# Optimization experiments

Hardware: AMD Instinct MI355X
Metric: run time of the kernel (lower is better)

The kernel has to match this reference:

```python
import jax, jax.numpy as jnp
import numpy as np

N, E = 50000, 800000
F_IN, F_OUT, H, F_EDGE = 256, 32, 8, 5
LEAKY_SLOPE = 0.2


def setup_inputs() -> dict:
    key = jax.random.key(0)
    ks = jax.random.split(key, 6)
    x = jax.random.normal(ks[0], (N, F_IN), dtype=jnp.float32)
    edge_index = jax.random.randint(ks[1], (2, E), 0, N, dtype=jnp.int64)
    edge_attr = jax.random.normal(ks[2], (E, F_EDGE), dtype=jnp.float32)
    degree_src = jax.random.randint(ks[3], (E,), 0, 64, dtype=jnp.int64)
    # Xavier-uniform params
    lim_W = float(np.sqrt(6.0 / (F_IN + F_OUT)))
    W = jax.random.uniform(ks[4], (H, F_IN, F_OUT), minval=-lim_W, maxval=lim_W, dtype=jnp.float32)
    A = 2 * F_OUT + F_EDGE
    lim_a = float(np.sqrt(6.0 / (H + A)))
    a = jax.random.uniform(ks[5], (H, A), minval=-lim_a, maxval=lim_a, dtype=jnp.float32)
    lim_e = float(np.sqrt(1.0 / F_EDGE))
    W_edge_w = jax.random.uniform(jax.random.fold_in(key, 7), (F_EDGE, F_EDGE), minval=-lim_e, maxval=lim_e, dtype=jnp.float32)
    return {"x": x, "edge_index": edge_index, "edge_attr": edge_attr,
            "degree_src": degree_src, "W": W, "a": a, "W_edge_w": W_edge_w}


def reference(x, edge_index, edge_attr, degree_src, W, a, W_edge_w):
    n = x.shape[0]
    h, f_out = W.shape[0], W.shape[2]
    src, dst = edge_index[0], edge_index[1]
    # per-head projection: (N, H, F_out)
    Wh = jnp.einsum('nf,hfo->nho', x, W)
    # split attention vector instead of materializing the concat
    a_src, a_dst, a_e = a[:, :f_out], a[:, f_out:2 * f_out], a[:, 2 * f_out:]
    ef = edge_attr @ W_edge_w.T                      # (E, F_edge)
    e = (jnp.einsum('eho,ho->eh', Wh[src], a_src)
         + jnp.einsum('eho,ho->eh', Wh[dst], a_dst)
         + ef @ a_e.T)                                # (E, H)
    e = jax.nn.leaky_relu(e, LEAKY_SLOPE)
    scale = 1.0 / jnp.sqrt(jnp.clip(degree_src.astype(jnp.float32), 1.0, None))
    e = e * scale[:, None]
    # segment softmax over src; torch scatter_reduce amax include_self=True with zeros init -> max includes 0
    e_max = jnp.maximum(jax.ops.segment_max(e, src, num_segments=n), 0.0)
    e_exp = jnp.exp(e - e_max[src])
    e_sum = jax.ops.segment_sum(e_exp, src, num_segments=n)
    alpha = e_exp / (e_sum[src] + 1e-16)             # (E, H)
    msg = Wh[dst] * alpha[:, :, None]                # (E, H, F_out)
    out = jax.ops.segment_sum(msg, src, num_segments=n)
    out = jax.nn.elu(out.reshape(n, h * f_out))
    return out, alpha
```

## Files before the change

kernel.cpp:

```cpp
#include <hip/hip_runtime.h>
#include <hip/hip_bf16.h>
#include <math.h>

#define NN 50000
#define NE 800000
#define FIN 256
#define FOUT 32
#define NH 8
#define FE 5
#define AROW 69
#define NROWS_PAD 50048

typedef float f32x4 __attribute__((ext_vector_type(4)));
typedef short bf16x8 __attribute__((ext_vector_type(8)));

static __device__ __forceinline__ unsigned short f2bf(float f) {
    unsigned u = __float_as_uint(f);
    unsigned r = (u + 0x7FFFu + ((u >> 16) & 1u)) >> 16;
    return (unsigned short)r;
}
static __device__ __forceinline__ float bf2f(unsigned short b) {
    return __uint_as_float(((unsigned)b) << 16);
}

__global__ __launch_bounds__(256) void k_prep(const float* __restrict__ W,
                                              const float* __restrict__ a,
                                              const float* __restrict__ Wew,
                                              float* __restrict__ C,
                                              unsigned short* __restrict__ Bh,
                                              unsigned short* __restrict__ Bl,
                                              unsigned short* __restrict__ Bsh,
                                              unsigned short* __restrict__ Bsl) {
    int t = threadIdx.x;
    if (blockIdx.x == 0) {
        if (t < NH * FE) {
            int h = t / FE, k = t % FE;
            float s = 0.f;
            for (int j = 0; j < FE; ++j) s += a[h * AROW + 2 * FOUT + j] * Wew[j * FE + k];
            C[t] = s;
        }
        int k = t;
        for (int h = 0; h < NH; ++h) {
            float s1v = 0.f, s2v = 0.f;
            for (int o = 0; o < FOUT; ++o) {
                float wv = W[(size_t)h * (FIN * FOUT) + (size_t)k * FOUT + o];
                s1v += wv * a[h * AROW + o];
                s2v += wv * a[h * AROW + FOUT + o];
            }
            unsigned short h1 = f2bf(s1v);
            Bsh[h * 256 + k] = h1;
            Bsl[h * 256 + k] = f2bf(s1v - bf2f(h1));
            unsigned short h2 = f2bf(s2v);
            Bsh[(8 + h) * 256 + k] = h2;
            Bsl[(8 + h) * 256 + k] = f2bf(s2v - bf2f(h2));
        }
    } else {
        int c = blockIdx.x - 1;
        int k = t;
        int h = c >> 5, o = c & 31;
        float f = W[(size_t)h * (FIN * FOUT) + (size_t)k * FOUT + o];
        unsigned short hi = f2bf(f);
        unsigned short lo = f2bf(f - bf2f(hi));
        Bh[c * 256 + k] = hi;
        Bl[c * 256 + k] = lo;
    }
}

__global__ __launch_bounds__(256) void k_pre2(const float* __restrict__ x,
                                              unsigned short* __restrict__ xb,
                                              const int* __restrict__ ei,
                                              int* __restrict__ counts,
                                              int* __restrict__ pos) {
    int i = blockIdx.x * 256 + threadIdx.x;
    if (i < (NN * FIN) / 8) {
        f32x4 u0 = *(const f32x4*)&x[(size_t)i * 8];
        f32x4 u1 = *(const f32x4*)&x[(size_t)i * 8 + 4];
        bf16x8 hi;
        hi[0] = (short)f2bf(u0.x); hi[1] = (short)f2bf(u0.y);
        hi[2] = (short)f2bf(u0.z); hi[3] = (short)f2bf(u0.w);
        hi[4] = (short)f2bf(u1.x); hi[5] = (short)f2bf(u1.y);
        hi[6] = (short)f2bf(u1.z); hi[7] = (short)f2bf(u1.w);
        *(bf16x8*)&xb[(size_t)i * 8] = hi;
    }
    if (i < NE / 4) {
        int4 e4 = *(const int4*)&ei[i * 4];
        int4 pv;
        pv.x = atomicAdd(&counts[e4.x], 1);
        pv.y = atomicAdd(&counts[e4.y], 1);
        pv.z = atomicAdd(&counts[e4.z], 1);
        pv.w = atomicAdd(&counts[e4.w], 1);
        *(int4*)&pos[i * 4] = pv;
    }
}

__global__ __launch_bounds__(256) void k_gemm_mfma(const unsigned short* __restrict__ xb,
                                                   const unsigned short* __restrict__ Bh,
                                                   const unsigned short* __restrict__ Bl,
                                                   const unsigned short* __restrict__ Bsh,
                                                   const unsigned short* __restrict__ Bsl,
                                                   unsigned short* __restrict__ Whb,
                                                   float* __restrict__ s1,
                                                   float* __restrict__ s2, int nrows) {
    int t = threadIdx.x;
    int w = t >> 6, l = t & 63;
    int r = l & 15, blk = l >> 4;
    int row0 = blockIdx.x * 64;
    int c0 = w * 64;

    f32x4 acc[4][4];
    f32x4 acc_s = (f32x4)(0.f);
#pragma unroll
    for (int i = 0; i < 4; ++i)
#pragma unroll
        for (int j = 0; j < 4; ++j) acc[i][j] = (f32x4)(0.f);

    const unsigned short* ap[4];
#pragma unroll
    for (int rt = 0; rt < 4; ++rt)
        ap[rt] = xb + (size_t)(row0 + rt * 16 + r) * 256 + blk * 8;

#pragma unroll
    for (int ks = 0; ks < 8; ++ks) {
        const int k0 = ks * 32;
        bf16x8 ah[4];
#pragma unroll
        for (int rt = 0; rt < 4; ++rt)
            ah[rt] = *(const bf16x8*)(ap[rt] + k0);
        bf16x8 bh[4], bl[4];
#pragma unroll
        for (int ct = 0; ct < 4; ++ct) {
            int c = c0 + ct * 16 + r;
            bh[ct] = *(const bf16x8*)&Bh[c * 256 + k0 + blk * 8];
            bl[ct] = *(const bf16x8*)&Bl[c * 256 + k0 + blk * 8];
        }
        bf16x8 bsh = *(const bf16x8*)&Bsh[r * 256 + k0 + blk * 8];
        bf16x8 bsl = *(const bf16x8*)&Bsl[r * 256 + k0 + blk * 8];
#pragma unroll
        for (int ct = 0; ct < 4; ++ct) {
#pragma unroll
            for (int rt = 0; rt < 4; ++rt) {
                acc[rt][ct] = __builtin_amdgcn_mfma_f32_16x16x32_bf16(ah[rt], bh[ct], acc[rt][ct], 0, 0, 0);
                acc[rt][ct] = __builtin_amdgcn_mfma_f32_16x16x32_bf16(ah[rt], bl[ct], acc[rt][ct], 0, 0, 0);
            }
        }
        acc_s = __builtin_amdgcn_mfma_f32_16x16x32_bf16(ah[w], bsh, acc_s, 0, 0, 0);
        acc_s = __builtin_amdgcn_mfma_f32_16x16x32_bf16(ah[w], bsl, acc_s, 0, 0, 0);
    }

#pragma unroll
    for (int rt = 0; rt < 4; ++rt) {
#pragma unroll
        for (int reg = 0; reg < 4; ++reg) {
            int row = row0 + rt * 16 + blk * 4 + reg;
            if (row < nrows) {
#pragma unroll
                for (int ct = 0; ct < 4; ++ct)
                    Whb[(size_t)row * 256 + c0 + ct * 16 + r] = f2bf(acc[rt][ct][reg]);
            }
        }
    }
#pragma unroll
    for (int reg = 0; reg < 4; ++reg) {
        int row = row0 + w * 16 + blk * 4 + reg;
        if (row < nrows) {
            if (r < 8) s1[row * NH + r] = acc_s[reg];
            else       s2[row * NH + (r - 8)] = acc_s[reg];
        }
    }
}

__global__ __launch_bounds__(256) void k_scanA(const int* __restrict__ counts,
                                               int* __restrict__ part,
                                               int* __restrict__ bsums, int n) {
    __shared__ int lds[256];
    int t = threadIdx.x;
    int base = blockIdx.x * 1024;
    int i0 = base + t * 4;
    int v0 = (i0 + 0 < n) ? counts[i0 + 0] : 0;
    int v1 = (i0 + 1 < n) ? counts[i0 + 1] : 0;
    int v2 = (i0 + 2 < n) ? counts[i0 + 2] : 0;
    int v3 = (i0 + 3 < n) ? counts[i0 + 3] : 0;
    int l0 = v0, l1 = l0 + v1, l2 = l1 + v2, l3 = l2 + v3;
    lds[t] = l3;
    __syncthreads();
    for (int off = 1; off < 256; off <<= 1) {
        int val = lds[t];
        if (t >= off) val += lds[t - off];
        __syncthreads();
        lds[t] = val;
        __syncthreads();
    }
    int excl = (t == 0) ? 0 : lds[t - 1];
    if (i0 + 0 < n) part[i0 + 0] = excl;
    if (i0 + 1 < n) part[i0 + 1] = excl + l0;
    if (i0 + 2 < n) part[i0 + 2] = excl + l1;
    if (i0 + 3 < n) part[i0 + 3] = excl + l2;
    if (t == 255) bsums[blockIdx.x] = lds[255];
}

__global__ void k_scanB(const int* __restrict__ bsums, int* __restrict__ boffs, int nb) {
    __shared__ int s[64];
    int t = threadIdx.x;
    int v = (t < nb) ? bsums[t] : 0;
    s[t] = v;
    __syncthreads();
    for (int off = 1; off < 64; off <<= 1) {
        int x = s[t];
        if (t >= off) x += s[t - off];
        __syncthreads();
        s[t] = x;
        __syncthreads();
    }
    if (t < nb) boffs[t] = s[t] - v;
}

__global__ __launch_bounds__(256) void k_scanC(int* __restrict__ row_ptr,
                                               const int* __restrict__ boffs, int n, int total) {
    int i = blockIdx.x * 256 + threadIdx.x;
    if (i < n) row_ptr[i] += boffs[i >> 10];
    else if (i == n) row_ptr[n] = total;
}

__global__ __launch_bounds__(256) void k_scatlog(const int* __restrict__ ei,
                                                 const float* __restrict__ eattr,
                                                 const int* __restrict__ degs,
                                                 const float* __restrict__ s1,
                                                 const float* __restrict__ s2,
                                                 const float* __restrict__ C,
                                                 const int* __restrict__ row_ptr,
                                                 const int* __restrict__ pos,
                                                 unsigned short* __restrict__ e_perm,
                                                 int2* __restrict__ de_perm) {
    __shared__ float Cl[NH * FE];
    int t = threadIdx.x;
    if (t < NH * FE) Cl[t] = C[t];
    __syncthreads();
    int e = blockIdx.x * 256 + t;
    if (e >= NE) return;
    int src = ei[e], dst = ei[NE + e];
    int dg = degs[e];
    float scale = rsqrtf((float)(dg > 1 ? dg : 1));
    float ea0 = eattr[(size_t)e * FE + 0];
    float ea1 = eattr[(size_t)e * FE + 1];
    float ea2 = eattr[(size_t)e * FE + 2];
    float ea3 = eattr[(size_t)e * FE + 3];
    float ea4 = eattr[(size_t)e * FE + 4];
    float4 s1a = *(const float4*)&s1[src * NH];
    float4 s1b = *(const float4*)&s1[src * NH + 4];
    float4 s2a = *(const float4*)&s2[dst * NH];
    float4 s2b = *(const float4*)&s2[dst * NH + 4];
    float vs1[8] = {s1a.x, s1a.y, s1a.z, s1a.w, s1b.x, s1b.y, s1b.z, s1b.w};
    float vs2[8] = {s2a.x, s2a.y, s2a.z, s2a.w, s2b.x, s2b.y, s2b.z, s2b.w};
    bf16x8 v;
#pragma unroll
    for (int h = 0; h < NH; ++h) {
        float q = vs1[h] + vs2[h] + ea0 * Cl[h * FE + 0] + ea1 * Cl[h * FE + 1] +
                  ea2 * Cl[h * FE + 2] + ea3 * Cl[h * FE + 3] + ea4 * Cl[h * FE + 4];
        q = q > 0.f ? q : 0.2f * q;
        v[h] = (short)f2bf(q * scale);
    }
    int p = row_ptr[src] + pos[e];
    *(bf16x8*)&e_perm[(size_t)p * 8] = v;
    de_perm[p] = make_int2(dst, e);
}

__global__ __launch_bounds__(256) void k_smmsg(const int* __restrict__ row_ptr,
                                               const unsigned short* __restrict__ e_perm,
                                               const int2* __restrict__ de_perm,
                                               const unsigned short* __restrict__ Whb,
                                               float* __restrict__ out_alpha,
                                               float* __restrict__ out) {
    __shared__ float al[4][256];
    __shared__ int dl[4][32];
    __shared__ int el[4][32];
    int t = threadIdx.x;
    int w = t >> 6, l = t & 63;
    int n = blockIdx.x * 4 + w;
    if (n >= NN) return;
    int start = row_ptr[n], deg = row_ptr[n + 1] - start;
    int j = l >> 3, h = l & 7;

    float vc[4];
#pragma unroll
    for (int q = 0; q < 4; ++q) {
        int b = j + 8 * q;
        vc[q] = (b < deg) ? bf2f(e_perm[(size_t)(start + b) * 8 + h]) : -1e30f;
    }
    float mx = 0.f;
#pragma unroll
    for (int q = 0; q < 4; ++q) mx = fmaxf(mx, vc[q]);
    for (int b = 32 + j; b < deg; b += 8)
        mx = fmaxf(mx, bf2f(e_perm[(size_t)(start + b) * 8 + h]));
    mx = fmaxf(mx, __shfl_xor(mx, 8));
    mx = fmaxf(mx, __shfl_xor(mx, 16));
    mx = fmaxf(mx, __shfl_xor(mx, 32));
    float m = mx;
    float ex[4];
    float sm = 0.f;
#pragma unroll
    for (int q = 0; q < 4; ++q) { ex[q] = __expf(vc[q] - m); sm += ex[q]; }
    for (int b = 32 + j; b < deg; b += 8)
        sm += __expf(bf2f(e_perm[(size_t)(start + b) * 8 + h]) - m);
    sm += __shfl_xor(sm, 8);
    sm += __shfl_xor(sm, 16);
    sm += __shfl_xor(sm, 32);
    float inv = 1.f / (sm + 1e-16f);
    f32x4 acc = (f32x4)(0.f);
    int hh = l >> 3;
    for (int base = 0; base < deg; base += 32) {
        int cnt = deg - base;
        if (cnt > 32) cnt = 32;
        if (l < cnt) {
            int2 de = de_perm[start + base + l];
            dl[w][l] = de.x;
            el[w][l] = de.y;
        }
        asm volatile("s_waitcnt lgkmcnt(0)" ::: "memory");
#pragma unroll
        for (int q = 0; q < 4; ++q) {
            int b = base + j + 8 * q;
            if (b < deg) {
                float av = (base == 0 ? ex[q]
                                      : __expf(bf2f(e_perm[(size_t)(start + b) * 8 + h]) - m)) * inv;
                al[w][(j + 8 * q) * 8 + h] = av;
                out_alpha[(size_t)el[w][j + 8 * q] * 8 + h] = av;
            }
        }
        asm volatile("s_waitcnt lgkmcnt(0)" ::: "memory");
        for (int jj = 0; jj < cnt; ++jj) {
            int d = dl[w][jj];
            float av = al[w][jj * 8 + hh];
            ushort4 u = *(const ushort4*)&Whb[(size_t)d * 256 + l * 4];
            acc.x += av * bf2f(u.x);
            acc.y += av * bf2f(u.y);
            acc.z += av * bf2f(u.z);
            acc.w += av * bf2f(u.w);
        }
        asm volatile("s_waitcnt lgkmcnt(0)" ::: "memory");
    }
    f32x4 o;
    o.x = acc.x > 0.f ? acc.x : expm1f(acc.x);
    o.y = acc.y > 0.f ? acc.y : expm1f(acc.y);
    o.z = acc.z > 0.f ? acc.z : expm1f(acc.z);
    o.w = acc.w > 0.f ? acc.w : expm1f(acc.w);
    *(f32x4*)&out[(size_t)n * 256 + l * 4] = o;
}

extern "C" void kernel_launch(void* const* d_in, const int* in_sizes, int n_in,
                              void* d_out, int out_size, void* d_ws, size_t ws_size,
                              hipStream_t stream) {
    const float* x     = (const float*)d_in[0];
    const int*   ei    = (const int*)d_in[1];
    const float* eattr = (const float*)d_in[2];
    const int*   degs  = (const int*)d_in[3];
    const float* W     = (const float*)d_in[4];
    const float* a     = (const float*)d_in[5];
    const float* Wew   = (const float*)d_in[6];

    float* out       = (float*)d_out;
    float* out_alpha = out + (size_t)NN * 256;

    char* p = (char*)d_ws;
    auto alloc = [&](size_t bytes) -> char* {
        char* r = p;
        p += (bytes + 255) & ~(size_t)255;
        return r;
    };
    unsigned short* Whb     = (unsigned short*)alloc((size_t)NN * 256 * 2);
    unsigned short* xb      = (unsigned short*)alloc((size_t)NROWS_PAD * 256 * 2);
    float*          s1      = (float*)alloc((size_t)NN * NH * 4);
    float*          s2      = (float*)alloc((size_t)NN * NH * 4);
    float*          Cm      = (float*)alloc(NH * FE * 4);
    unsigned short* Bh      = (unsigned short*)alloc((size_t)256 * 256 * 2);
    unsigned short* Bl      = (unsigned short*)alloc((size_t)256 * 256 * 2);
    unsigned short* Bsh     = (unsigned short*)alloc((size_t)16 * 256 * 2);
    unsigned short* Bsl     = (unsigned short*)alloc((size_t)16 * 256 * 2);
    int*            counts  = (int*)alloc((size_t)NN * 4);
    int*            row_ptr = (int*)alloc((size_t)(NN + 1) * 4);
    int*            bsums   = (int*)alloc(64 * 4);
    int*            boffs   = (int*)alloc(64 * 4);
    int*            pos     = (int*)alloc((size_t)NE * 4);
    unsigned short* e_perm  = (unsigned short*)alloc((size_t)NE * NH * 2);
    int2*           de_perm = (int2*)alloc((size_t)NE * 8);

    hipMemsetAsync(counts, 0, (size_t)NN * 4, stream);

    k_prep<<<257, 256, 0, stream>>>(W, a, Wew, Cm, Bh, Bl, Bsh, Bsl);
    k_pre2<<<(NN * FIN / 8 + 255) / 256, 256, 0, stream>>>(x, xb, ei, counts, pos);
    k_gemm_mfma<<<(NN + 63) / 64, 256, 0, stream>>>(xb, Bh, Bl, Bsh, Bsl, Whb, s1, s2, NN);
    k_scanA<<<(NN + 1023) / 1024, 256, 0, stream>>>(counts, row_ptr, bsums, NN);
    k_scanB<<<1, 64, 0, stream>>>(bsums, boffs, (NN + 1023) / 1024);
    k_scanC<<<(NN + 1 + 255) / 256, 256, 0, stream>>>(row_ptr, boffs, NN, NE);
    k_scatlog<<<(NE + 255) / 256, 256, 0, stream>>>(ei, eattr, degs, s1, s2, Cm,
                                                    row_ptr, pos, e_perm, de_perm);
    k_smmsg<<<(NN + 3) / 4, 256, 0, stream>>>(row_ptr, e_perm, de_perm, Whb,
                                              out_alpha, out);
}
```

Before: 254.9 us.

## Drop bf16 low-part GEMM, fuse prep kernels, single-pass scan, unroll gather

Removes the bf16 hi/lo split for W so the projection GEMM issues half as many MFMAs and skips loading and writing the low-part buffer. Merges the weight-prep and x-conversion/count kernels into one launch. Replaces the three-kernel scan with one kernel whose blocks publish their totals through flags and spin-wait on earlier blocks. Unrolls the message gather loop by two. Projection precision drops to plain bf16 for W, and the spin-wait assumes all scan blocks are resident at the same time.

Result: faster. 235.2 us (-7.7%).

```diff
diff --git a/kernel.cpp b/kernel.cpp
--- a/kernel.cpp
+++ b/kernel.cpp
@@ -23,16 +23,44 @@
     return __uint_as_float(((unsigned)b) << 16);
 }
 
-__global__ __launch_bounds__(256) void k_prep(const float* __restrict__ W,
-                                              const float* __restrict__ a,
-                                              const float* __restrict__ Wew,
-                                              float* __restrict__ C,
-                                              unsigned short* __restrict__ Bh,
-                                              unsigned short* __restrict__ Bl,
-                                              unsigned short* __restrict__ Bsh,
-                                              unsigned short* __restrict__ Bsl) {
-    int t = threadIdx.x;
-    if (blockIdx.x == 0) {
+__global__ __launch_bounds__(256) void k_prepre(const float* __restrict__ W,
+                                                const float* __restrict__ a,
+                                                const float* __restrict__ Wew,
+                                                const float* __restrict__ x,
+                                                const int* __restrict__ ei,
+                                                float* __restrict__ C,
+                                                unsigned short* __restrict__ Bh,
+                                                unsigned short* __restrict__ Bsh,
+                                                unsigned short* __restrict__ Bsl,
+                                                unsigned short* __restrict__ xb,
+                                                int* __restrict__ counts,
+                                                int* __restrict__ pos) {
+    int b = blockIdx.x, t = threadIdx.x;
+    int i = b * 256 + t;
+    if (i < (NN * FIN) / 8) {
+        f32x4 u0 = *(const f32x4*)&x[(size_t)i * 8];
+        f32x4 u1 = *(const f32x4*)&x[(size_t)i * 8 + 4];
+        bf16x8 hi;
+        hi[0] = (short)f2bf(u0.x); hi[1] = (short)f2bf(u0.y);
+        hi[2] = (short)f2bf(u0.z); hi[3] = (short)f2bf(u0.w);
+        hi[4] = (short)f2bf(u1.x); hi[5] = (short)f2bf(u1.y);
+        hi[6] = (short)f2bf(u1.z); hi[7] = (short)f2bf(u1.w);
+        *(bf16x8*)&xb[(size_t)i * 8] = hi;
+    }
+    if (i < NE / 4) {
+        int4 e4 = *(const int4*)&ei[i * 4];
+        int4 pv;
+        pv.x = atomicAdd(&counts[e4.x], 1);
+        pv.y = atomicAdd(&counts[e4.y], 1);
+        pv.z = atomicAdd(&counts[e4.z], 1);
+        pv.w = atomicAdd(&counts[e4.w], 1);
+        *(int4*)&pos[i * 4] = pv;
+    }
+    if (b < 256) {
+        int c = b, k = t;
+        int h = c >> 5, o = c & 31;
+        Bh[c * 256 + k] = f2bf(W[(size_t)h * (FIN * FOUT) + (size_t)k * FOUT + o]);
+    } else if (b == 256) {
         if (t < NH * FE) {
             int h = t / FE, k = t % FE;
             float s = 0.f;
@@ -54,48 +82,11 @@
             Bsh[(8 + h) * 256 + k] = h2;
             Bsl[(8 + h) * 256 + k] = f2bf(s2v - bf2f(h2));
         }
-    } else {
-        int c = blockIdx.x - 1;
-        int k = t;
-        int h = c >> 5, o = c & 31;
-        float f = W[(size_t)h * (FIN * FOUT) + (size_t)k * FOUT + o];
-        unsigned short hi = f2bf(f);
-        unsigned short lo = f2bf(f - bf2f(hi));
-        Bh[c * 256 + k] = hi;
-        Bl[c * 256 + k] = lo;
-    }
-}
-
-__global__ __launch_bounds__(256) void k_pre2(const float* __restrict__ x,
-                                              unsigned short* __restrict__ xb,
-                                              const int* __restrict__ ei,
-                                              int* __restrict__ counts,
-                                              int* __restrict__ pos) {
-    int i = blockIdx.x * 256 + threadIdx.x;
-    if (i < (NN * FIN) / 8) {
-        f32x4 u0 = *(const f32x4*)&x[(size_t)i * 8];
-        f32x4 u1 = *(const f32x4*)&x[(size_t)i * 8 + 4];
-        bf16x8 hi;
-        hi[0] = (short)f2bf(u0.x); hi[1] = (short)f2bf(u0.y);
-        hi[2] = (short)f2bf(u0.z); hi[3] = (short)f2bf(u0.w);
-        hi[4] = (short)f2bf(u1.x); hi[5] = (short)f2bf(u1.y);
-        hi[6] = (short)f2bf(u1.z); hi[7] = (short)f2bf(u1.w);
-        *(bf16x8*)&xb[(size_t)i * 8] = hi;
-    }
-    if (i < NE / 4) {
-        int4 e4 = *(const int4*)&ei[i * 4];
-        int4 pv;
-        pv.x = atomicAdd(&counts[e4.x], 1);
-        pv.y = atomicAdd(&counts[e4.y], 1);
-        pv.z = atomicAdd(&counts[e4.z], 1);
-        pv.w = atomicAdd(&counts[e4.w], 1);
-        *(int4*)&pos[i * 4] = pv;
     }
 }
 
 __global__ __launch_bounds__(256) void k_gemm_mfma(const unsigned short* __restrict__ xb,
                                                    const unsigned short* __restrict__ Bh,
-                                                   const unsigned short* __restrict__ Bl,
                                                    const unsigned short* __restrict__ Bsh,
                                                    const unsigned short* __restrict__ Bsl,
                                                    unsigned short* __restrict__ Whb,
@@ -126,22 +117,19 @@
 #pragma unroll
         for (int rt = 0; rt < 4; ++rt)
             ah[rt] = *(const bf16x8*)(ap[rt] + k0);
-        bf16x8 bh[4], bl[4];
+        bf16x8 bh[4];
 #pragma unroll
         for (int ct = 0; ct < 4; ++ct) {
             int c = c0 + ct * 16 + r;
             bh[ct] = *(const bf16x8*)&Bh[c * 256 + k0 + blk * 8];
-            bl[ct] = *(const bf16x8*)&Bl[c * 256 + k0 + blk * 8];
         }
         bf16x8 bsh = *(const bf16x8*)&Bsh[r * 256 + k0 + blk * 8];
         bf16x8 bsl = *(const bf16x8*)&Bsl[r * 256 + k0 + blk * 8];
 #pragma unroll
         for (int ct = 0; ct < 4; ++ct) {
 #pragma unroll
-            for (int rt = 0; rt < 4; ++rt) {
+            for (int rt = 0; rt < 4; ++rt)
                 acc[rt][ct] = __builtin_amdgcn_mfma_f32_16x16x32_bf16(ah[rt], bh[ct], acc[rt][ct], 0, 0, 0);
-                acc[rt][ct] = __builtin_amdgcn_mfma_f32_16x16x32_bf16(ah[rt], bl[ct], acc[rt][ct], 0, 0, 0);
-            }
         }
         acc_s = __builtin_amdgcn_mfma_f32_16x16x32_bf16(ah[w], bsh, acc_s, 0, 0, 0);
         acc_s = __builtin_amdgcn_mfma_f32_16x16x32_bf16(ah[w], bsl, acc_s, 0, 0, 0);
@@ -169,13 +157,12 @@
     }
 }
 
-__global__ __launch_bounds__(256) void k_scanA(const int* __restrict__ counts,
-                                               int* __restrict__ part,
-                                               int* __restrict__ bsums, int n) {
+__global__ __launch_bounds__(256) void k_scan(const int* __restrict__ counts,
+                                              int* __restrict__ row_ptr,
+                                              int* __restrict__ bflag, int n, int total_edges) {
     __shared__ int lds[256];
-    int t = threadIdx.x;
-    int base = blockIdx.x * 1024;
-    int i0 = base + t * 4;
+    int t = threadIdx.x, bid = blockIdx.x;
+    int i0 = bid * 1024 + t * 4;
     int v0 = (i0 + 0 < n) ? counts[i0 + 0] : 0;
     int v1 = (i0 + 1 < n) ? counts[i0 + 1] : 0;
     int v2 = (i0 + 2 < n) ? counts[i0 + 2] : 0;
@@ -191,34 +178,27 @@
         __syncthreads();
     }
     int excl = (t == 0) ? 0 : lds[t - 1];
-    if (i0 + 0 < n) part[i0 + 0] = excl;
-    if (i0 + 1 < n) part[i0 + 1] = excl + l0;
-    if (i0 + 2 < n) part[i0 + 2] = excl + l1;
-    if (i0 + 3 < n) part[i0 + 3] = excl + l2;
-    if (t == 255) bsums[blockIdx.x] = lds[255];
-}
-
-__global__ void k_scanB(const int* __restrict__ bsums, int* __restrict__ boffs, int nb) {
-    __shared__ int s[64];
-    int t = threadIdx.x;
-    int v = (t < nb) ? bsums[t] : 0;
-    s[t] = v;
+    int total = lds[255];
     __syncthreads();
-    for (int off = 1; off < 64; off <<= 1) {
-        int x = s[t];
-        if (t >= off) x += s[t - off];
+    if (t == 0) atomicExch(&bflag[bid], total + 1);
+    int myv = 0;
+    if (t < bid) {
+        int v;
+        do { v = atomicAdd(&bflag[t], 0); } while (v == 0);
+        myv = v - 1;
+    }
+    lds[t] = myv;
+    __syncthreads();
+    for (int off = 128; off > 0; off >>= 1) {
+        if (t < off) lds[t] += lds[t + off];
         __syncthreads();
-        s[t] = x;
-        __syncthreads();
-    }
-    if (t < nb) boffs[t] = s[t] - v;
-}
-
-__global__ __launch_bounds__(256) void k_scanC(int* __restrict__ row_ptr,
-                                               const int* __restrict__ boffs, int n, int total) {
-    int i = blockIdx.x * 256 + threadIdx.x;
-    if (i < n) row_ptr[i] += boffs[i >> 10];
-    else if (i == n) row_ptr[n] = total;
+    }
+    int gbase = lds[0];
+    if (i0 + 0 < n) row_ptr[i0 + 0] = gbase + excl;
+    if (i0 + 1 < n) row_ptr[i0 + 1] = gbase + excl + l0;
+    if (i0 + 2 < n) row_ptr[i0 + 2] = gbase + excl + l1;
+    if (i0 + 3 < n) row_ptr[i0 + 3] = gbase + excl + l2;
+    if (bid == gridDim.x - 1 && t == 255) row_ptr[n] = total_edges;
 }
 
 __global__ __launch_bounds__(256) void k_scatlog(const int* __restrict__ ei,
@@ -327,14 +307,25 @@
             }
         }
         asm volatile("s_waitcnt lgkmcnt(0)" ::: "memory");
-        for (int jj = 0; jj < cnt; ++jj) {
-            int d = dl[w][jj];
-            float av = al[w][jj * 8 + hh];
-            ushort4 u = *(const ushort4*)&Whb[(size_t)d * 256 + l * 4];
-            acc.x += av * bf2f(u.x);
-            acc.y += av * bf2f(u.y);
-            acc.z += av * bf2f(u.z);
-            acc.w += av * bf2f(u.w);
+        int jj = 0;
+        for (; jj + 2 <= cnt; jj += 2) {
+            int d0 = dl[w][jj], d1 = dl[w][jj + 1];
+            float a0 = al[w][jj * 8 + hh], a1 = al[w][jj * 8 + 8 + hh];
+            ushort4 u0 = *(const ushort4*)&Whb[(size_t)d0 * 256 + l * 4];
+            ushort4 u1 = *(const ushort4*)&Whb[(size_t)d1 * 256 + l * 4];
+            acc.x += a0 * bf2f(u0.x) + a1 * bf2f(u1.x);
+            acc.y += a0 * bf2f(u0.y) + a1 * bf2f(u1.y);
+            acc.z += a0 * bf2f(u0.z) + a1 * bf2f(u1.z);
+            acc.w += a0 * bf2f(u0.w) + a1 * bf2f(u1.w);
+        }
+        if (jj < cnt) {
+            int d0 = dl[w][jj];
+            float a0 = al[w][jj * 8 + hh];
+            ushort4 u0 = *(const ushort4*)&Whb[(size_t)d0 * 256 + l * 4];
+            acc.x += a0 * bf2f(u0.x);
+            acc.y += a0 * bf2f(u0.y);
+            acc.z += a0 * bf2f(u0.z);
+            acc.w += a0 * bf2f(u0.w);
         }
         asm volatile("s_waitcnt lgkmcnt(0)" ::: "memory");
     }
@@ -372,25 +363,21 @@
     float*          s2      = (float*)alloc((size_t)NN * NH * 4);
     float*          Cm      = (float*)alloc(NH * FE * 4);
     unsigned short* Bh      = (unsigned short*)alloc((size_t)256 * 256 * 2);
-    unsigned short* Bl      = (unsigned short*)alloc((size_t)256 * 256 * 2);
     unsigned short* Bsh     = (unsigned short*)alloc((size_t)16 * 256 * 2);
     unsigned short* Bsl     = (unsigned short*)alloc((size_t)16 * 256 * 2);
-    int*            counts  = (int*)alloc((size_t)NN * 4);
+    int*            counts  = (int*)alloc((size_t)(NN + 64) * 4);
+    int*            bflag   = counts + NN;
     int*            row_ptr = (int*)alloc((size_t)(NN + 1) * 4);
-    int*            bsums   = (int*)alloc(64 * 4);
-    int*            boffs   = (int*)alloc(64 * 4);
     int*            pos     = (int*)alloc((size_t)NE * 4);
     unsigned short* e_perm  = (unsigned short*)alloc((size_t)NE * NH * 2);
     int2*           de_perm = (int2*)alloc((size_t)NE * 8);
 
-    hipMemsetAsync(counts, 0, (size_t)NN * 4, stream);
-
-    k_prep<<<257, 256, 0, stream>>>(W, a, Wew, Cm, Bh, Bl, Bsh, Bsl);
-    k_pre2<<<(NN * FIN / 8 + 255) / 256, 256, 0, stream>>>(x, xb, ei, counts, pos);
-    k_gemm_mfma<<<(NN + 63) / 64, 256, 0, stream>>>(xb, Bh, Bl, Bsh, Bsl, Whb, s1, s2, NN);
-    k_scanA<<<(NN + 1023) / 1024, 256, 0, stream>>>(counts, row_ptr, bsums, NN);
-    k_scanB<<<1, 64, 0, stream>>>(bsums, boffs, (NN + 1023) / 1024);
-    k_scanC<<<(NN + 1 + 255) / 256, 256, 0, stream>>>(row_ptr, boffs, NN, NE);
+    hipMemsetAsync(counts, 0, (size_t)(NN + 64) * 4, stream);
+
+    k_prepre<<<(NN * FIN / 8 + 255) / 256, 256, 0, stream>>>(W, a, Wew, x, ei, Cm, Bh,
+                                                             Bsh, Bsl, xb, counts, pos);
+    k_gemm_mfma<<<(NN + 63) / 64, 256, 0, stream>>>(xb, Bh, Bsh, Bsl, Whb, s1, s2, NN);
+    k_scan<<<(NN + 1023) / 1024, 256, 0, stream>>>(counts, row_ptr, bflag, NN, NE);
     k_scatlog<<<(NE + 255) / 256, 256, 0, stream>>>(ei, eattr, degs, s1, s2, Cm,
                                                     row_ptr, pos, e_perm, de_perm);
     k_smmsg<<<(NN + 3) / 4, 256, 0, stream>>>(row_ptr, e_perm, de_perm, Whb,
```
